# Performance work log

Measured on AMD Instinct MI355X. Metric: run time of the kernel, lower is better.

## Reference

```python
import jax, jax.numpy as jnp
import numpy as np

NUM_HEADS = 16
WINDOW = 256  # window_size: each query i attends to keys [max(0, i-W+1), i]


def setup_inputs() -> dict:
    key = jax.random.key(0)
    k1, k2, k3, k4, k5 = jax.random.split(key, 5)
    B, S, D = 2, 4096, 1024
    scale = 0.02
    return {
        "x": jax.random.normal(k1, (B, S, D), dtype=jnp.float32),
        "wq": jax.random.normal(k2, (D, D), dtype=jnp.float32) * scale,
        "wk": jax.random.normal(k3, (D, D), dtype=jnp.float32) * scale,
        "wv": jax.random.normal(k4, (D, D), dtype=jnp.float32) * scale,
        "wo": jax.random.normal(k5, (D, D), dtype=jnp.float32) * scale,
    }


def _sliding_window_attn(x, wq, wk, wv, wo):
    B, S, D = x.shape
    H, W = NUM_HEADS, WINDOW
    Dh = D // H
    nb = S // W  # number of query blocks (S assumed divisible by W)

    def proj(w):
        # nn.Linear: y = x @ w.T ; -> [B, H, nb, W, Dh]
        y = (x @ w.T).reshape(B, nb, W, H, Dh)
        return y.transpose(0, 3, 1, 2, 4)

    q = proj(wq)
    k = proj(wk)
    v = proj(wv)

    # Each query block j attends to key blocks j-1 and j (banded causal window).
    zpad = jnp.zeros((B, H, 1, W, Dh), dtype=x.dtype)
    kpad = jnp.concatenate([zpad, k], axis=2)  # [B,H,nb+1,W,Dh]
    vpad = jnp.concatenate([zpad, v], axis=2)
    k2 = jnp.concatenate([kpad[:, :, :-1], kpad[:, :, 1:]], axis=3)  # [B,H,nb,2W,Dh]
    v2 = jnp.concatenate([vpad[:, :, :-1], vpad[:, :, 1:]], axis=3)

    scores = jnp.einsum("bhjqd,bhjkd->bhjqk", q, k2) / jnp.sqrt(
        jnp.asarray(Dh, dtype=x.dtype)
    )  # [B,H,nb,W,2W]

    # Mask: query global pos i = j*W + qi; key global pos kp = (j-1)*W + ki.
    # Valid iff i-W+1 <= kp <= i  <=>  qi+1 <= ki <= qi+W ; and kp >= 0.
    qi = jnp.arange(W)[:, None]          # [W,1]
    ki = jnp.arange(2 * W)[None, :]      # [1,2W]
    band = (ki >= qi + 1) & (ki <= qi + W)                      # [W,2W]
    kpos_ok = (jnp.arange(nb)[:, None, None] - 1) * W + ki[None] >= 0  # [nb,1,2W]
    mask = band[None] & kpos_ok          # [nb,W,2W]

    neg = jnp.finfo(scores.dtype).min
    scores = jnp.where(mask[None, None], scores, neg)
    attn = jax.nn.softmax(scores, axis=-1)

    out = jnp.einsum("bhjqk,bhjkd->bhjqd", attn, v2)  # [B,H,nb,W,Dh]
    out = out.transpose(0, 2, 3, 1, 4).reshape(B, S, D)
    return out @ wo.T


def reference(x, wq, wk, wv, wo):
    return _sliding_window_attn(x, wq, wk, wv, wo)
```

## Files before the change

kernel.cpp:

```cpp
#include <hip/hip_runtime.h>

#define S_LEN 4096
#define DMODEL 1024
#define NH 16
#define DH 64
#define WIN 256
#define NQKV 3072

typedef __attribute__((ext_vector_type(8))) short short8;
typedef __attribute__((ext_vector_type(4))) short sh4;
typedef __attribute__((ext_vector_type(4))) float floatx4;

__device__ __forceinline__ ushort f2bf(float f) {
    union { float f; unsigned int i; } x;
    x.f = f;
    unsigned int r = x.i + 0x7FFFu + ((x.i >> 16) & 1u);
    return (ushort)(r >> 16);
}

__global__ __launch_bounds__(256) void cvt_all(const float* __restrict__ x,
                                               const float* __restrict__ wq,
                                               const float* __restrict__ wk,
                                               const float* __restrict__ wv,
                                               const float* __restrict__ wo,
                                               ushort* __restrict__ xb,
                                               ushort* __restrict__ W3b,
                                               ushort* __restrict__ wob,
                                               int nx8, int nw8) {
    int i = blockIdx.x * 256 + threadIdx.x;
    const float* src;
    ushort* dst;
    if (i < nx8) {
        src = x + (size_t)i * 8;            dst = xb + (size_t)i * 8;
    } else {
        int j = i - nx8;
        int which = j / nw8, r = j - which * nw8;
        if (which >= 4) return;
        const float* w4[4] = {wq, wk, wv, wo};
        src = w4[which] + (size_t)r * 8;
        dst = (which == 3 ? wob : W3b + (size_t)which * nw8 * 8) + (size_t)r * 8;
    }
    floatx4 f0 = *(const floatx4*)src;
    floatx4 f1 = *(const floatx4*)(src + 4);
    short8 v;
#pragma unroll
    for (int e = 0; e < 4; ++e) v[e] = (short)f2bf(f0[e]);
#pragma unroll
    for (int e = 0; e < 4; ++e) v[4 + e] = (short)f2bf(f1[e]);
    *(short8*)dst = v;
}

template <bool OUTF32>
__global__ __launch_bounds__(256) void gemm_bf16(const ushort* __restrict__ A,
                                                 const ushort* __restrict__ W,
                                                 void* __restrict__ Cout,
                                                 int M, int N, int K) {
    __shared__ __align__(16) ushort As[128 * 32];
    __shared__ __align__(16) ushort Ws[128 * 32];

    const int tid = threadIdx.x;
    const int w = tid >> 6, l = tid & 63;
    const int bm0 = blockIdx.y * 128, bn0 = blockIdx.x * 128;
    const int wm = (w >> 1) * 64, wn = (w & 1) * 64;
    const int lm = l & 15, quad = l >> 4;

    floatx4 acc[4][4] = {};

    const int row0 = tid >> 2, col0 = (tid & 3) * 8;
    const ushort* a0 = A + (size_t)(bm0 + row0) * K + col0;
    const ushort* a1 = A + (size_t)(bm0 + row0 + 64) * K + col0;
    const ushort* w0 = W + (size_t)(bn0 + row0) * K + col0;
    const ushort* w1 = W + (size_t)(bn0 + row0 + 64) * K + col0;

    for (int k0 = 0; k0 < K; k0 += 32) {
        __builtin_amdgcn_global_load_lds(
            (const __attribute__((address_space(1))) void*)(a0 + k0),
            (__attribute__((address_space(3))) void*)(As + tid * 8), 16, 0, 0);
        __builtin_amdgcn_global_load_lds(
            (const __attribute__((address_space(1))) void*)(a1 + k0),
            (__attribute__((address_space(3))) void*)(As + 2048 + tid * 8), 16, 0, 0);
        __builtin_amdgcn_global_load_lds(
            (const __attribute__((address_space(1))) void*)(w0 + k0),
            (__attribute__((address_space(3))) void*)(Ws + tid * 8), 16, 0, 0);
        __builtin_amdgcn_global_load_lds(
            (const __attribute__((address_space(1))) void*)(w1 + k0),
            (__attribute__((address_space(3))) void*)(Ws + 2048 + tid * 8), 16, 0, 0);
        __syncthreads();

        short8 af[4], wf[4];
#pragma unroll
        for (int mi = 0; mi < 4; ++mi)
            af[mi] = *(const short8*)&As[(wm + mi * 16 + lm) * 32 + quad * 8];
#pragma unroll
        for (int ni = 0; ni < 4; ++ni)
            wf[ni] = *(const short8*)&Ws[(wn + ni * 16 + lm) * 32 + quad * 8];
#pragma unroll
        for (int mi = 0; mi < 4; ++mi)
#pragma unroll
            for (int ni = 0; ni < 4; ++ni)
                acc[mi][ni] = __builtin_amdgcn_mfma_f32_16x16x32_bf16(
                    af[mi], wf[ni], acc[mi][ni], 0, 0, 0);
        __syncthreads();
    }

#pragma unroll
    for (int mi = 0; mi < 4; ++mi)
#pragma unroll
        for (int ni = 0; ni < 4; ++ni)
#pragma unroll
            for (int r = 0; r < 4; ++r) {
                int row = bm0 + wm + mi * 16 + quad * 4 + r;
                int col = bn0 + wn + ni * 16 + lm;
                if (OUTF32)
                    ((float*)Cout)[(size_t)row * N + col] = acc[mi][ni][r];
                else
                    ((ushort*)Cout)[(size_t)row * N + col] = f2bf(acc[mi][ni][r]);
            }
}

template <bool OUTF32>
__global__ __launch_bounds__(256, 2) void gemm_qkv(const ushort* __restrict__ A,
                                                   const ushort* __restrict__ W,
                                                   void* __restrict__ Cout,
                                                   int M, int N, int K) {
    __shared__ __align__(16) ushort As[128 * 64];
    __shared__ __align__(16) ushort Ws[256 * 64];

    const int tid = threadIdx.x;
    const int w = tid >> 6, l = tid & 63;
    const int bm0 = blockIdx.y * 128, bn0 = blockIdx.x * 256;
    const int wm = (w >> 1) * 64, wn = (w & 1) * 128;
    const int lm = l & 15, quad = l >> 4;

    floatx4 acc[4][8] = {};

    int arow[4], acol[4];
#pragma unroll
    for (int p = 0; p < 4; ++p) {
        int c = p * 256 + tid;
        arow[p] = c >> 3;
        acol[p] = (((c & 7) ^ (arow[p] & 7))) * 8;
    }
    int wrow[8], wcol[8];
#pragma unroll
    for (int p = 0; p < 8; ++p) {
        int c = p * 256 + tid;
        wrow[p] = c >> 3;
        wcol[p] = (((c & 7) ^ (wrow[p] & 7))) * 8;
    }

    for (int k0 = 0; k0 < K; k0 += 64) {
#pragma unroll
        for (int p = 0; p < 4; ++p)
            __builtin_amdgcn_global_load_lds(
                (const __attribute__((address_space(1))) void*)
                    (A + (size_t)(bm0 + arow[p]) * K + k0 + acol[p]),
                (__attribute__((address_space(3))) void*)(As + p * 2048 + tid * 8),
                16, 0, 0);
#pragma unroll
        for (int p = 0; p < 8; ++p)
            __builtin_amdgcn_global_load_lds(
                (const __attribute__((address_space(1))) void*)
                    (W + (size_t)(bn0 + wrow[p]) * K + k0 + wcol[p]),
                (__attribute__((address_space(3))) void*)(Ws + p * 2048 + tid * 8),
                16, 0, 0);
        __syncthreads();

#pragma unroll
        for (int kk = 0; kk < 2; ++kk) {
            const int sseg = ((kk * 4 + quad) ^ (lm & 7)) * 8;
            short8 af[4], wf[8];
#pragma unroll
            for (int mi = 0; mi < 4; ++mi)
                af[mi] = *(const short8*)&As[(wm + mi * 16 + lm) * 64 + sseg];
#pragma unroll
            for (int ni = 0; ni < 8; ++ni)
                wf[ni] = *(const short8*)&Ws[(wn + ni * 16 + lm) * 64 + sseg];
#pragma unroll
            for (int mi = 0; mi < 4; ++mi)
#pragma unroll
                for (int ni = 0; ni < 8; ++ni)
                    acc[mi][ni] = __builtin_amdgcn_mfma_f32_16x16x32_bf16(
                        af[mi], wf[ni], acc[mi][ni], 0, 0, 0);
        }
        __syncthreads();
    }

#pragma unroll
    for (int mi = 0; mi < 4; ++mi)
#pragma unroll
        for (int ni = 0; ni < 8; ++ni)
#pragma unroll
            for (int r = 0; r < 4; ++r) {
                int row = bm0 + wm + mi * 16 + quad * 4 + r;
                int col = bn0 + wn + ni * 16 + lm;
                if (OUTF32)
                    ((float*)Cout)[(size_t)row * N + col] = acc[mi][ni][r];
                else
                    ((ushort*)Cout)[(size_t)row * N + col] = f2bf(acc[mi][ni][r]);
            }
}

#define KSP 72
#define VTP 136
#define PSP 40

__global__ __launch_bounds__(256) void swattn_mfma(const ushort* __restrict__ QKV,
                                                   ushort* __restrict__ O) {
    __shared__ __align__(16) ushort Ks[128 * KSP];
    __shared__ __align__(16) ushort Vt[64 * VTP];
    __shared__ __align__(16) ushort Ps[2][4 * 64 * PSP];
    __shared__ __align__(16) float lW[256];

    const int j = blockIdx.x, h = blockIdx.y, b = blockIdx.z;
    const int tid = threadIdx.x;
    const int w = tid >> 6, l = tid & 63;
    const int quad = l >> 4, lc = l & 15;

    const size_t base = (size_t)b * S_LEN * NQKV + (size_t)h * DH;
    const ushort* Qp = QKV + base;
    const ushort* Kp = QKV + base + DMODEL;
    const ushort* Vp = QKV + base + 2 * DMODEL;

    short8 qf[4][2];
#pragma unroll
    for (int nq = 0; nq < 4; ++nq)
#pragma unroll
        for (int kk = 0; kk < 2; ++kk)
            qf[nq][kk] = *(const short8*)(Qp +
                (size_t)(j * 256 + w * 64 + nq * 16 + lc) * NQKV + kk * 32 + quad * 8);

    floatx4 o[4][4] = {};
    float lsum[4] = {0.f, 0.f, 0.f, 0.f};

    const float sscale = 0.18033688011112042f;
    const float M0 = 2.0f;
    const int qlo = w * 64, qhi = w * 64 + 63;

    for (int c = 0; c < 4; ++c) {
        const int kg0 = (j - 1) * 256 + c * 128;
        if (kg0 < 0) continue;
        __syncthreads();
#pragma unroll
        for (int i = 0; i < 4; ++i) {
            int cc = i * 256 + tid, key = cc >> 3, seg = cc & 7;
            *(short8*)&Ks[key * KSP + seg * 8] =
                *(const short8*)(Kp + (size_t)(kg0 + key) * NQKV + seg * 8);
            short8 vv = *(const short8*)(Vp + (size_t)(kg0 + key) * NQKV + seg * 8);
#pragma unroll
            for (int e = 0; e < 8; ++e)
                Vt[(e * 8 + seg) * VTP + key] = (ushort)vv[e];
        }
        __syncthreads();

        const int krel0 = c * 128 - 256;
#pragma unroll
        for (int g = 0; g < 4; ++g) {
            const int k0 = krel0 + g * 32;
            if (k0 > qhi || k0 + 31 < qlo - 255) continue;
            ushort* Pw = &Ps[g & 1][w * 64 * PSP];

            floatx4 st[2][4];
            const floatx4 zero = {};
#pragma unroll
            for (int kt = 0; kt < 2; ++kt) {
                short8 kf0 = *(const short8*)&Ks[(g * 32 + kt * 16 + lc) * KSP + quad * 8];
                short8 kf1 = *(const short8*)&Ks[(g * 32 + kt * 16 + lc) * KSP + 32 + quad * 8];
#pragma unroll
                for (int nq = 0; nq < 4; ++nq) {
                    int kmin = k0 + kt * 16, qmin = qlo + nq * 16;
                    if (kmin > qmin + 15 || kmin + 270 < qmin) {
                        st[kt][nq] = zero;
                        continue;
                    }
                    st[kt][nq] = __builtin_amdgcn_mfma_f32_16x16x32_bf16(kf0, qf[nq][0], zero, 0, 0, 0);
                    st[kt][nq] = __builtin_amdgcn_mfma_f32_16x16x32_bf16(kf1, qf[nq][1], st[kt][nq], 0, 0, 0);
                }
            }
#pragma unroll
            for (int kt = 0; kt < 2; ++kt)
#pragma unroll
                for (int nq = 0; nq < 4; ++nq) {
                    sh4 pv;
                    int kmin = k0 + kt * 16, qmin = qlo + nq * 16;
                    if (kmin > qmin + 15 || kmin + 270 < qmin) {
                        pv[0] = pv[1] = pv[2] = pv[3] = 0;
                    } else if (kmin + 15 <= qmin && kmin + 240 >= qmin) {
#pragma unroll
                        for (int r = 0; r < 4; ++r) {
                            float p = exp2f(st[kt][nq][r] * sscale - M0);
                            lsum[nq] += p;
                            pv[r] = (short)f2bf(p);
                        }
                    } else {
#pragma unroll
                        for (int r = 0; r < 4; ++r) {
                            int krel = kmin + quad * 4 + r;
                            int qrel = qmin + lc;
                            bool valid = (krel <= qrel) && (krel + 255 >= qrel);
                            float p = valid ? exp2f(st[kt][nq][r] * sscale - M0) : 0.f;
                            lsum[nq] += p;
                            pv[r] = (short)f2bf(p);
                        }
                    }
                    *(sh4*)&Pw[(nq * 16 + lc) * PSP + kt * 16 + quad * 4] = pv;
                }
            __threadfence_block();

            short8 vf[4];
#pragma unroll
            for (int nd = 0; nd < 4; ++nd) {
                int prow = (lc & 7) * 8 + nd * 2 + (lc >> 3);
                vf[nd] = *(const short8*)&Vt[prow * VTP + g * 32 + quad * 8];
            }
#pragma unroll
            for (int mq = 0; mq < 4; ++mq) {
                int qmin = qlo + mq * 16;
                if (k0 > qmin + 15 || k0 + 286 < qmin) continue;
                short8 pf = *(const short8*)&Pw[(mq * 16 + lc) * PSP + quad * 8];
#pragma unroll
                for (int nd = 0; nd < 4; ++nd)
                    o[mq][nd] = __builtin_amdgcn_mfma_f32_16x16x32_bf16(pf, vf[nd], o[mq][nd], 0, 0, 0);
            }
        }
    }

#pragma unroll
    for (int nq = 0; nq < 4; ++nq) {
        lsum[nq] += __shfl_xor(lsum[nq], 16);
        lsum[nq] += __shfl_xor(lsum[nq], 32);
    }
    if (l < 16) {
#pragma unroll
        for (int nq = 0; nq < 4; ++nq) lW[w * 64 + nq * 16 + l] = lsum[nq];
    }
    __threadfence_block();
#pragma unroll
    for (int mq = 0; mq < 4; ++mq) {
        floatx4 lv = *(const floatx4*)&lW[w * 64 + mq * 16 + quad * 4];
#pragma unroll
        for (int r = 0; r < 4; ++r) {
            float inv = 1.f / lv[r];
            int token = j * 256 + w * 64 + mq * 16 + quad * 4 + r;
#pragma unroll
            for (int nd = 0; nd < 4; ++nd)
                O[(size_t)b * S_LEN * DMODEL + (size_t)token * DMODEL + h * DH + nd * 16 + lc] =
                    f2bf(o[mq][nd][r] * inv);
        }
    }
}

extern "C" void kernel_launch(void* const* d_in, const int* in_sizes, int n_in,
                              void* d_out, int out_size, void* d_ws, size_t ws_size,
                              hipStream_t stream) {
    const float* x  = (const float*)d_in[0];
    const float* wq = (const float*)d_in[1];
    const float* wk = (const float*)d_in[2];
    const float* wv = (const float*)d_in[3];
    const float* wo = (const float*)d_in[4];
    float* out = (float*)d_out;

    const int D = DMODEL;
    const int M = in_sizes[0] / D;
    const int Bb = M / S_LEN;

    ushort* xb   = (ushort*)d_ws;
    ushort* W3b  = xb + (size_t)M * D;
    ushort* wob  = W3b + (size_t)NQKV * D;
    ushort* QKVb = wob + (size_t)D * D;
    ushort* Ob   = xb;

    const int nx8 = M * D / 8, nw8 = D * D / 8;
    const int ntot = nx8 + 4 * nw8;
    cvt_all<<<dim3((ntot + 255) / 256), dim3(256), 0, stream>>>(
        x, wq, wk, wv, wo, xb, W3b, wob, nx8, nw8);

    gemm_qkv<false><<<dim3(NQKV / 256, M / 128), dim3(256), 0, stream>>>(
        xb, W3b, QKVb, M, NQKV, D);

    swattn_mfma<<<dim3(S_LEN / WIN, NH, Bb), dim3(256), 0, stream>>>(QKVb, Ob);

    gemm_bf16<true><<<dim3(D / 128, M / 128), dim3(256), 0, stream>>>(
        Ob, wob, out, M, D, D);
}
```

Baseline: 229.0 us.

## Unify GEMMs on 128x256 tile kernel with XCD remap; read K fragments directly

Merges the two GEMM kernels into one 128x256-tile, K=64-step swizzled-LDS kernel and uses it for the output projection too, replacing the old 128x128, K=32 tile. Adds a block-index remap that groups row-tiles per XCD, meant to improve L2 locality. The attention kernel no longer stages K in shared memory and loads K fragments straight from global memory, saving LDS and a staging pass at the cost of uncoalesced global reads. The output projection now launches only 4x64 blocks, which may underfill the GPU.

Result: no change. 229.7 us (+0.3%).

```diff
diff --git a/kernel.cpp b/kernel.cpp
--- a/kernel.cpp
+++ b/kernel.cpp
@@ -50,164 +50,108 @@
     *(short8*)dst = v;
 }
 
+#define GLOAD16(src, dst)                                                     \
+    __builtin_amdgcn_global_load_lds(                                         \
+        (const __attribute__((address_space(1))) void*)(src),                 \
+        (__attribute__((address_space(3))) void*)(dst), 16, 0, 0)
+
 template <bool OUTF32>
-__global__ __launch_bounds__(256) void gemm_bf16(const ushort* __restrict__ A,
-                                                 const ushort* __restrict__ W,
-                                                 void* __restrict__ Cout,
-                                                 int M, int N, int K) {
-    __shared__ __align__(16) ushort As[128 * 32];
-    __shared__ __align__(16) ushort Ws[128 * 32];
+__global__ __launch_bounds__(256, 2) void gemm128(const ushort* __restrict__ A,
+                                                  const ushort* __restrict__ W,
+                                                  void* __restrict__ Cout,
+                                                  int M, int N, int K) {
+    __shared__ __align__(16) ushort As[128 * 64];
+    __shared__ __align__(16) ushort Ws[256 * 64];
 
     const int tid = threadIdx.x;
     const int w = tid >> 6, l = tid & 63;
-    const int bm0 = blockIdx.y * 128, bn0 = blockIdx.x * 128;
-    const int wm = (w >> 1) * 64, wn = (w & 1) * 64;
+
+    int bx, by;
+    {
+        const int nbx = gridDim.x, nby = gridDim.y;
+        if ((nby & 7) == 0) {
+            const int lin = blockIdx.y * nbx + blockIdx.x;
+            const int rpb = nby >> 3;
+            const int xcd = lin & 7, idx = lin >> 3;
+            bx = idx / rpb;
+            by = xcd * rpb + (idx - bx * rpb);
+        } else {
+            bx = blockIdx.x;
+            by = blockIdx.y;
+        }
+    }
+    const int bm0 = by * 128, bn0 = bx * 256;
+    const int wm = (w >> 1) * 64, wn = (w & 1) * 128;
     const int lm = l & 15, quad = l >> 4;
 
-    floatx4 acc[4][4] = {};
-
-    const int row0 = tid >> 2, col0 = (tid & 3) * 8;
-    const ushort* a0 = A + (size_t)(bm0 + row0) * K + col0;
-    const ushort* a1 = A + (size_t)(bm0 + row0 + 64) * K + col0;
-    const ushort* w0 = W + (size_t)(bn0 + row0) * K + col0;
-    const ushort* w1 = W + (size_t)(bn0 + row0 + 64) * K + col0;
-
-    for (int k0 = 0; k0 < K; k0 += 32) {
-        __builtin_amdgcn_global_load_lds(
-            (const __attribute__((address_space(1))) void*)(a0 + k0),
-            (__attribute__((address_space(3))) void*)(As + tid * 8), 16, 0, 0);
-        __builtin_amdgcn_global_load_lds(
-            (const __attribute__((address_space(1))) void*)(a1 + k0),
-            (__attribute__((address_space(3))) void*)(As + 2048 + tid * 8), 16, 0, 0);
-        __builtin_amdgcn_global_load_lds(
-            (const __attribute__((address_space(1))) void*)(w0 + k0),
-            (__attribute__((address_space(3))) void*)(Ws + tid * 8), 16, 0, 0);
-        __builtin_amdgcn_global_load_lds(
-            (const __attribute__((address_space(1))) void*)(w1 + k0),
-            (__attribute__((address_space(3))) void*)(Ws + 2048 + tid * 8), 16, 0, 0);
+    floatx4 acc[4][8] = {};
+
+    int arow[4], acol[4];
+#pragma unroll
+    for (int p = 0; p < 4; ++p) {
+        int c = p * 256 + tid;
+        arow[p] = c >> 3;
+        acol[p] = (((c & 7) ^ (arow[p] & 7))) * 8;
+    }
+    int wrow[8], wcol[8];
+#pragma unroll
+    for (int p = 0; p < 8; ++p) {
+        int c = p * 256 + tid;
+        wrow[p] = c >> 3;
+        wcol[p] = (((c & 7) ^ (wrow[p] & 7))) * 8;
+    }
+
+    for (int k0 = 0; k0 < K; k0 += 64) {
+#pragma unroll
+        for (int p = 0; p < 4; ++p)
+            GLOAD16(A + (size_t)(bm0 + arow[p]) * K + k0 + acol[p],
+                    As + p * 2048 + tid * 8);
+#pragma unroll
+        for (int p = 0; p < 8; ++p)
+            GLOAD16(W + (size_t)(bn0 + wrow[p]) * K + k0 + wcol[p],
+                    Ws + p * 2048 + tid * 8);
         __syncthreads();
 
-        short8 af[4], wf[4];
-#pragma unroll
-        for (int mi = 0; mi < 4; ++mi)
-            af[mi] = *(const short8*)&As[(wm + mi * 16 + lm) * 32 + quad * 8];
-#pragma unroll
-        for (int ni = 0; ni < 4; ++ni)
-            wf[ni] = *(const short8*)&Ws[(wn + ni * 16 + lm) * 32 + quad * 8];
-#pragma unroll
-        for (int mi = 0; mi < 4; ++mi)
-#pragma unroll
-            for (int ni = 0; ni < 4; ++ni)
-                acc[mi][ni] = __builtin_amdgcn_mfma_f32_16x16x32_bf16(
-                    af[mi], wf[ni], acc[mi][ni], 0, 0, 0);
+#pragma unroll
+        for (int kk = 0; kk < 2; ++kk) {
+            const int sseg = ((kk * 4 + quad) ^ (lm & 7)) * 8;
+            short8 af[4], wf[8];
+#pragma unroll
+            for (int mi = 0; mi < 4; ++mi)
+                af[mi] = *(const short8*)&As[(wm + mi * 16 + lm) * 64 + sseg];
+#pragma unroll
+            for (int ni = 0; ni < 8; ++ni)
+                wf[ni] = *(const short8*)&Ws[(wn + ni * 16 + lm) * 64 + sseg];
+#pragma unroll
+            for (int mi = 0; mi < 4; ++mi)
+#pragma unroll
+                for (int ni = 0; ni < 8; ++ni)
+                    acc[mi][ni] = __builtin_amdgcn_mfma_f32_16x16x32_bf16(
+                        af[mi], wf[ni], acc[mi][ni], 0, 0, 0);
+        }
         __syncthreads();
     }
 
 #pragma unroll
     for (int mi = 0; mi < 4; ++mi)
 #pragma unroll
-        for (int ni = 0; ni < 4; ++ni)
+        for (int ni = 0; ni < 8; ++ni)
 #pragma unroll
             for (int r = 0; r < 4; ++r) {
                 int row = bm0 + wm + mi * 16 + quad * 4 + r;
                 int col = bn0 + wn + ni * 16 + lm;
-                if (OUTF32)
+                if constexpr (OUTF32)
                     ((float*)Cout)[(size_t)row * N + col] = acc[mi][ni][r];
                 else
                     ((ushort*)Cout)[(size_t)row * N + col] = f2bf(acc[mi][ni][r]);
             }
 }
 
-template <bool OUTF32>
-__global__ __launch_bounds__(256, 2) void gemm_qkv(const ushort* __restrict__ A,
-                                                   const ushort* __restrict__ W,
-                                                   void* __restrict__ Cout,
-                                                   int M, int N, int K) {
-    __shared__ __align__(16) ushort As[128 * 64];
-    __shared__ __align__(16) ushort Ws[256 * 64];
-
-    const int tid = threadIdx.x;
-    const int w = tid >> 6, l = tid & 63;
-    const int bm0 = blockIdx.y * 128, bn0 = blockIdx.x * 256;
-    const int wm = (w >> 1) * 64, wn = (w & 1) * 128;
-    const int lm = l & 15, quad = l >> 4;
-
-    floatx4 acc[4][8] = {};
-
-    int arow[4], acol[4];
-#pragma unroll
-    for (int p = 0; p < 4; ++p) {
-        int c = p * 256 + tid;
-        arow[p] = c >> 3;
-        acol[p] = (((c & 7) ^ (arow[p] & 7))) * 8;
-    }
-    int wrow[8], wcol[8];
-#pragma unroll
-    for (int p = 0; p < 8; ++p) {
-        int c = p * 256 + tid;
-        wrow[p] = c >> 3;
-        wcol[p] = (((c & 7) ^ (wrow[p] & 7))) * 8;
-    }
-
-    for (int k0 = 0; k0 < K; k0 += 64) {
-#pragma unroll
-        for (int p = 0; p < 4; ++p)
-            __builtin_amdgcn_global_load_lds(
-                (const __attribute__((address_space(1))) void*)
-                    (A + (size_t)(bm0 + arow[p]) * K + k0 + acol[p]),
-                (__attribute__((address_space(3))) void*)(As + p * 2048 + tid * 8),
-                16, 0, 0);
-#pragma unroll
-        for (int p = 0; p < 8; ++p)
-            __builtin_amdgcn_global_load_lds(
-                (const __attribute__((address_space(1))) void*)
-                    (W + (size_t)(bn0 + wrow[p]) * K + k0 + wcol[p]),
-                (__attribute__((address_space(3))) void*)(Ws + p * 2048 + tid * 8),
-                16, 0, 0);
-        __syncthreads();
-
-#pragma unroll
-        for (int kk = 0; kk < 2; ++kk) {
-            const int sseg = ((kk * 4 + quad) ^ (lm & 7)) * 8;
-            short8 af[4], wf[8];
-#pragma unroll
-            for (int mi = 0; mi < 4; ++mi)
-                af[mi] = *(const short8*)&As[(wm + mi * 16 + lm) * 64 + sseg];
-#pragma unroll
-            for (int ni = 0; ni < 8; ++ni)
-                wf[ni] = *(const short8*)&Ws[(wn + ni * 16 + lm) * 64 + sseg];
-#pragma unroll
-            for (int mi = 0; mi < 4; ++mi)
-#pragma unroll
-                for (int ni = 0; ni < 8; ++ni)
-                    acc[mi][ni] = __builtin_amdgcn_mfma_f32_16x16x32_bf16(
-                        af[mi], wf[ni], acc[mi][ni], 0, 0, 0);
-        }
-        __syncthreads();
-    }
-
-#pragma unroll
-    for (int mi = 0; mi < 4; ++mi)
-#pragma unroll
-        for (int ni = 0; ni < 8; ++ni)
-#pragma unroll
-            for (int r = 0; r < 4; ++r) {
-                int row = bm0 + wm + mi * 16 + quad * 4 + r;
-                int col = bn0 + wn + ni * 16 + lm;
-                if (OUTF32)
-                    ((float*)Cout)[(size_t)row * N + col] = acc[mi][ni][r];
-                else
-                    ((ushort*)Cout)[(size_t)row * N + col] = f2bf(acc[mi][ni][r]);
-            }
-}
-
-#define KSP 72
 #define VTP 136
 #define PSP 40
 
 __global__ __launch_bounds__(256) void swattn_mfma(const ushort* __restrict__ QKV,
                                                    ushort* __restrict__ O) {
-    __shared__ __align__(16) ushort Ks[128 * KSP];
     __shared__ __align__(16) ushort Vt[64 * VTP];
     __shared__ __align__(16) ushort Ps[2][4 * 64 * PSP];
     __shared__ __align__(16) float lW[256];
@@ -244,8 +188,6 @@
 #pragma unroll
         for (int i = 0; i < 4; ++i) {
             int cc = i * 256 + tid, key = cc >> 3, seg = cc & 7;
-            *(short8*)&Ks[key * KSP + seg * 8] =
-                *(const short8*)(Kp + (size_t)(kg0 + key) * NQKV + seg * 8);
             short8 vv = *(const short8*)(Vp + (size_t)(kg0 + key) * NQKV + seg * 8);
 #pragma unroll
             for (int e = 0; e < 8; ++e)
@@ -264,8 +206,9 @@
             const floatx4 zero = {};
 #pragma unroll
             for (int kt = 0; kt < 2; ++kt) {
-                short8 kf0 = *(const short8*)&Ks[(g * 32 + kt * 16 + lc) * KSP + quad * 8];
-                short8 kf1 = *(const short8*)&Ks[(g * 32 + kt * 16 + lc) * KSP + 32 + quad * 8];
+                const ushort* Kr = Kp + (size_t)(kg0 + g * 32 + kt * 16 + lc) * NQKV;
+                short8 kf0 = *(const short8*)(Kr + quad * 8);
+                short8 kf1 = *(const short8*)(Kr + 32 + quad * 8);
 #pragma unroll
                 for (int nq = 0; nq < 4; ++nq) {
                     int kmin = k0 + kt * 16, qmin = qlo + nq * 16;
@@ -375,11 +318,11 @@
     cvt_all<<<dim3((ntot + 255) / 256), dim3(256), 0, stream>>>(
         x, wq, wk, wv, wo, xb, W3b, wob, nx8, nw8);
 
-    gemm_qkv<false><<<dim3(NQKV / 256, M / 128), dim3(256), 0, stream>>>(
+    gemm128<false><<<dim3(NQKV / 256, M / 128), dim3(256), 0, stream>>>(
         xb, W3b, QKVb, M, NQKV, D);
 
     swattn_mfma<<<dim3(S_LEN / WIN, NH, Bb), dim3(256), 0, stream>>>(QKVb, Ob);
 
-    gemm_bf16<true><<<dim3(D / 128, M / 128), dim3(256), 0, stream>>>(
+    gemm128<true><<<dim3(D / 256, M / 128), dim3(256), 0, stream>>>(
         Ob, wob, out, M, D, D);
 }
```
